# Kernel tuning notes

Hardware: AMD Instinct MI355X
Metric: run time of the kernel (lower is better)

## Reference

```python
import jax, jax.numpy as jnp
import numpy as np

NUM_HEADS = 8
LN_EPS = 1e-6


def _layer_norm(x, gamma, beta):
    mu = jnp.mean(x, axis=-1, keepdims=True)
    var = jnp.mean(jnp.square(x - mu), axis=-1, keepdims=True)
    return (x - mu) / jnp.sqrt(var + LN_EPS) * gamma + beta


def setup_inputs() -> dict:
    key = jax.random.key(0)
    B, S, H, F = 4, 2048, 1024, 4096
    ks = jax.random.split(key, 12)
    scale = 1.0 / np.sqrt(H)
    x = jax.random.normal(ks[0], (B, S, H), dtype=jnp.float32)
    # additive padding mask: 1 where masked, 0 where attended
    mask = jax.random.randint(ks[1], (B, 1, 1, S), 0, 2).astype(jnp.float32)
    Wq = jax.random.normal(ks[2], (H, H), dtype=jnp.float32) * scale
    Wk = jax.random.normal(ks[3], (H, H), dtype=jnp.float32) * scale
    Wv = jax.random.normal(ks[4], (H, H), dtype=jnp.float32) * scale
    Wo = jax.random.normal(ks[5], (H, H), dtype=jnp.float32) * scale
    W1 = jax.random.normal(ks[6], (H, F), dtype=jnp.float32) * scale
    b1 = jnp.zeros((F,), dtype=jnp.float32)
    W2 = jax.random.normal(ks[7], (F, H), dtype=jnp.float32) * (1.0 / np.sqrt(F))
    b2 = jnp.zeros((H,), dtype=jnp.float32)
    gamma = jnp.ones((H,), dtype=jnp.float32)
    beta = jnp.zeros((H,), dtype=jnp.float32)
    return {"x": x, "mask": mask, "Wq": Wq, "Wk": Wk, "Wv": Wv, "Wo": Wo,
            "W1": W1, "b1": b1, "W2": W2, "b2": b2, "gamma": gamma, "beta": beta}


def reference(x, mask, Wq, Wk, Wv, Wo, W1, b1, W2, b2, gamma, beta):
    B, S, H = x.shape
    nh = NUM_HEADS
    d = H // nh

    def split_heads(t):
        return t.reshape(B, S, nh, d).transpose(0, 2, 1, 3)  # [B,nh,S,d]

    q = split_heads(x @ Wq)
    k = split_heads(x @ Wk)
    v = split_heads(x @ Wv)

    # FAITHFUL to source bug: score /= d**(-0.5)  ==  score * sqrt(d)
    scores = jnp.einsum('bhqd,bhkd->bhqk', q, k) * jnp.sqrt(jnp.float32(d))
    scores = scores + mask * (-1e9)
    attn = jax.nn.softmax(scores, axis=-1)
    ctx = jnp.einsum('bhqk,bhkd->bhqd', attn, v)
    ctx = ctx.transpose(0, 2, 1, 3).reshape(B, S, H)
    attn_out = ctx @ Wo

    # dropout = identity (eval mode)
    x = _layer_norm(x + attn_out, gamma, beta)
    ffn = jnp.maximum(x @ W1 + b1, 0.0) @ W2 + b2
    x = _layer_norm(x + ffn, gamma, beta)
    return x
```

## Files before the change

### kernel.cpp

```cpp
#include <hip/hip_runtime.h>


typedef __bf16 bf16;
typedef __bf16 bf16x4 __attribute__((ext_vector_type(4)));
typedef __bf16 bf16x8 __attribute__((ext_vector_type(8)));
typedef float  f32x4  __attribute__((ext_vector_type(4)));

#define MFMA16(a, b, c) __builtin_amdgcn_mfma_f32_16x16x32_bf16(a, b, c, 0, 0, 0)

typedef const __attribute__((address_space(1))) void* gas_cptr;
typedef __attribute__((address_space(3))) void* las_ptr;

__device__ __forceinline__ void g2l16(const void* g, void* l) {
    __builtin_amdgcn_global_load_lds((gas_cptr)g, (las_ptr)l, 16, 0, 0);
}

__device__ __forceinline__ uint b16bits(bf16 v) {
    union { bf16 h; unsigned short u; } cv; cv.h = v; return (uint)cv.u;
}

__device__ __forceinline__ int xcd_swz(int d, int nwg) {
    return (d & 7) * (nwg >> 3) + (d >> 3);
}

__global__ __launch_bounds__(256) void split_f32_k(
    const float* __restrict__ in, bf16* __restrict__ hi, bf16* __restrict__ lo)
{
    const long i = (long)blockIdx.x * 256 + threadIdx.x;
    const float4 v = *(const float4*)(in + i * 4);
    const float a[4] = {v.x, v.y, v.z, v.w};
    bf16x4 h, l;
#pragma unroll
    for (int j = 0; j < 4; j++) {
        h[j] = (bf16)a[j];
        l[j] = (bf16)(a[j] - (float)h[j]);
    }
    *(bf16x4*)(hi + i * 4) = h;
    *(bf16x4*)(lo + i * 4) = l;
}

__global__ __launch_bounds__(256) void mask_scan_k(
    const float* __restrict__ mask, unsigned short* __restrict__ cidx,
    int* __restrict__ nbuf)
{
    __shared__ int wsum[4];
    const int b = blockIdx.x, t = threadIdx.x;
    const int lane = t & 63, w = t >> 6;
    float m[8];
    *(float4*)&m[0] = *(const float4*)(mask + b * 2048 + t * 8);
    *(float4*)&m[4] = *(const float4*)(mask + b * 2048 + t * 8 + 4);
    int keep[8], cnt = 0;
#pragma unroll
    for (int j = 0; j < 8; j++) {
        keep[j] = (m[j] < 0.5f) ? 1 : 0;
        cnt += keep[j];
    }
    int pre = cnt;
#pragma unroll
    for (int off = 1; off < 64; off <<= 1) {
        const int nv = __shfl_up(pre, off);
        if (lane >= off) pre += nv;
    }
    if (lane == 63) wsum[w] = pre;
    __syncthreads();
    int base = 0;
    for (int i = 0; i < w; i++) base += wsum[i];
    const int total = wsum[0] + wsum[1] + wsum[2] + wsum[3];
    int p = base + pre - cnt;
#pragma unroll
    for (int j = 0; j < 8; j++)
        if (keep[j]) cidx[b * 2048 + (p++)] = (unsigned short)(t * 8 + j);
    for (int j = t; j < 2048; j += 256)
        if (j >= total) cidx[b * 2048 + j] = 0;
    if (t == 0) nbuf[b] = total;
}

__global__ __launch_bounds__(256) void transpose_f32_k(
    const float* __restrict__ in, bf16* __restrict__ out_hi, bf16* __restrict__ out_lo,
    int in_rs, int out_rs)
{
    __shared__ uint Th[64][33];
    __shared__ uint Tl[64][33];
    const long c0 = (long)blockIdx.x * 64;
    const long r0 = (long)blockIdx.y * 64;
    const int t = threadIdx.x, rp = t >> 3, cc = t & 7;
    const float* pa = in + (r0 + 2 * rp) * (long)in_rs + c0 + cc * 8;
    const float* pb = pa + in_rs;
    float a[8], b[8];
    *(float4*)&a[0] = *(const float4*)pa;
    *(float4*)&a[4] = *(const float4*)(pa + 4);
    *(float4*)&b[0] = *(const float4*)pb;
    *(float4*)&b[4] = *(const float4*)(pb + 4);
#pragma unroll
    for (int j = 0; j < 8; j++) {
        const bf16 ah = (bf16)a[j], bh = (bf16)b[j];
        Th[cc * 8 + j][rp] = b16bits(ah) | (b16bits(bh) << 16);
        const bf16 al = (bf16)(a[j] - (float)ah), bl = (bf16)(b[j] - (float)bh);
        Tl[cc * 8 + j][rp] = b16bits(al) | (b16bits(bl) << 16);
    }
    __syncthreads();
#pragma unroll
    for (int i = 0; i < 2; i++) {
        const int task = i * 256 + t;
        const int c = task >> 3, ch = task & 7;
        uint4 wv;
        wv.x = Th[c][ch * 4 + 0]; wv.y = Th[c][ch * 4 + 1];
        wv.z = Th[c][ch * 4 + 2]; wv.w = Th[c][ch * 4 + 3];
        *(uint4*)(out_hi + (c0 + c) * (long)out_rs + r0 + ch * 8) = wv;
        if (out_lo) {
            uint4 wl;
            wl.x = Tl[c][ch * 4 + 0]; wl.y = Tl[c][ch * 4 + 1];
            wl.z = Tl[c][ch * 4 + 2]; wl.w = Tl[c][ch * 4 + 3];
            *(uint4*)(out_lo + (c0 + c) * (long)out_rs + r0 + ch * 8) = wl;
        }
    }
}

__global__ __launch_bounds__(256) void transpose_bf16_k(
    const bf16* __restrict__ in, bf16* __restrict__ out,
    int in_rs, int out_rs, int nh, long bo_in, long bi_in, long bo_out,
    const int* __restrict__ nbuf)
{
    __shared__ uint T[64][33];
    const int z = blockIdx.z;
    const int bb = z / nh;
    const long r0 = (long)blockIdx.y * 64;
    if (nbuf) {
        const int npad = (nbuf[bb] + 63) & ~63;
        if (r0 >= npad) return;
    }
    const bf16* inp = in + (long)bb * bo_in + (long)(z % nh) * bi_in;
    bf16* outp = out + (long)z * bo_out;
    const long c0 = (long)blockIdx.x * 64;
    const int t = threadIdx.x, rp = t >> 3, cc = t & 7;

    const uint4 ra = *(const uint4*)(inp + (r0 + 2 * rp) * (long)in_rs + c0 + cc * 8);
    const uint4 rb = *(const uint4*)(inp + (r0 + 2 * rp + 1) * (long)in_rs + c0 + cc * 8);
    const uint a32[4] = {ra.x, ra.y, ra.z, ra.w};
    const uint b32[4] = {rb.x, rb.y, rb.z, rb.w};
#pragma unroll
    for (int j = 0; j < 8; j++) {
        const uint av = (j & 1) ? (a32[j >> 1] >> 16) : (a32[j >> 1] & 0xffffu);
        const uint bv = (j & 1) ? (b32[j >> 1] >> 16) : (b32[j >> 1] & 0xffffu);
        T[cc * 8 + j][rp] = av | (bv << 16);
    }
    __syncthreads();
#pragma unroll
    for (int i = 0; i < 2; i++) {
        const int task = i * 256 + t;
        const int c = task >> 3, ch = task & 7;
        uint4 wv;
        wv.x = T[c][ch * 4 + 0]; wv.y = T[c][ch * 4 + 1];
        wv.z = T[c][ch * 4 + 2]; wv.w = T[c][ch * 4 + 3];
        *(uint4*)(outp + (c0 + c) * (long)out_rs + r0 + ch * 8) = wv;
    }
}

__global__ __launch_bounds__(256) void gemm_bf16_k(
    const bf16* __restrict__ A, const bf16* __restrict__ Bt,
    bf16* __restrict__ out,
    const float* __restrict__ bias, int relu, int M, int N, int K,
    const unsigned short* __restrict__ cidx, const int* __restrict__ nbuf)
{
    __shared__ __align__(16) bf16 As[128 * 32];
    __shared__ __align__(16) bf16 Bs[128 * 32];
    const int t = threadIdx.x;
    const int fr = t & 15, fq = (t >> 4) & 3;
    const int w = t >> 6, wm = w & 1, wn = w >> 1;
    const int nx = gridDim.x;
    const int d = xcd_swz(blockIdx.y * nx + blockIdx.x, nx * gridDim.y);
    const long mBase = (long)(d / nx) * 128;
    const long nBase = (long)(d % nx) * 128;

    const int arow = t >> 2;
    const int akc  = (t & 3) * 8;
    long r0 = mBase + arow, r1 = r0 + 64;
    if (cidx) {
        const int b = (int)(mBase >> 11);
        const int npad = (nbuf[b] + 63) & ~63;
        if ((int)(mBase & 2047) >= npad) return;
        r0 = (long)b * 2048 + cidx[b * 2048 + (int)(r0 & 2047)];
        r1 = (long)b * 2048 + cidx[b * 2048 + (int)(r1 & 2047)];
    }

    f32x4 acc[4][4];
#pragma unroll
    for (int i = 0; i < 4; i++)
#pragma unroll
        for (int j = 0; j < 4; j++) acc[i][j] = (f32x4){0.f, 0.f, 0.f, 0.f};

    const bf16* ga0 = A + r0 * (long)K + akc;
    const bf16* ga1 = A + r1 * (long)K + akc;
    const bf16* gb0 = Bt + (nBase + arow) * (long)K + akc;
    const bf16* gb1 = Bt + (nBase + arow + 64) * (long)K + akc;
    bf16* la0 = &As[t * 8];
    bf16* la1 = &As[(256 + t) * 8];
    bf16* lb0 = &Bs[t * 8];
    bf16* lb1 = &Bs[(256 + t) * 8];

    const int aoff = (wm * 64 + fr) * 32 + fq * 8;
    const int boff = (wn * 64 + fr) * 32 + fq * 8;

    for (int kt = 0; kt < K; kt += 32) {
        g2l16(ga0 + kt, la0);
        g2l16(ga1 + kt, la1);
        g2l16(gb0 + kt, lb0);
        g2l16(gb1 + kt, lb1);
        __syncthreads();
        bf16x8 af[4], bfv[4];
#pragma unroll
        for (int mt = 0; mt < 4; mt++) af[mt] = *(const bf16x8*)&As[aoff + mt * 512];
#pragma unroll
        for (int nt = 0; nt < 4; nt++) bfv[nt] = *(const bf16x8*)&Bs[boff + nt * 512];
#pragma unroll
        for (int mt = 0; mt < 4; mt++)
#pragma unroll
            for (int nt = 0; nt < 4; nt++)
                acc[mt][nt] = MFMA16(af[mt], bfv[nt], acc[mt][nt]);
        __syncthreads();
    }

    const long crow0 = mBase + wm * 64;
    const long ccol0 = nBase + wn * 64;
#pragma unroll
    for (int nt = 0; nt < 4; nt++) {
        const long col = ccol0 + nt * 16 + fr;
        const float bv = bias ? bias[col] : 0.0f;
#pragma unroll
        for (int mt = 0; mt < 4; mt++)
#pragma unroll
            for (int r = 0; r < 4; r++) {
                const long rowg = crow0 + mt * 16 + fq * 4 + r;
                float v = acc[mt][nt][r] + bv;
                if (relu) v = fmaxf(v, 0.0f);
                out[rowg * (long)N + col] = (bf16)v;
            }
    }
}

__global__ __launch_bounds__(256) void gemm_qk_split_k(
    const bf16* __restrict__ Ah, const bf16* __restrict__ Al,
    const bf16* __restrict__ BhQ, const bf16* __restrict__ BlQ,
    bf16* __restrict__ qhi, bf16* __restrict__ qlo,
    const bf16* __restrict__ BhK, const bf16* __restrict__ BlK,
    bf16* __restrict__ khi, bf16* __restrict__ klo,
    int M, int N, int K,
    const unsigned short* __restrict__ cidx, const int* __restrict__ nbuf)
{
    __shared__ __align__(16) bf16 Ahs[128 * 32];
    __shared__ __align__(16) bf16 Als[128 * 32];
    __shared__ __align__(16) bf16 Bhs[128 * 32];
    __shared__ __align__(16) bf16 Bls[128 * 32];
    const int t = threadIdx.x;
    const int fr = t & 15, fq = (t >> 4) & 3;
    const int w = t >> 6, wm = w & 1, wn = w >> 1;
    const int nx = gridDim.x;
    const int nxy = nx * gridDim.y;
    const int dAll = xcd_swz(blockIdx.z * nxy + blockIdx.y * nx + blockIdx.x, nxy * 2);
    const int z = dAll / nxy;
    const int d = dAll - z * nxy;
    const long mBase = (long)(d / nx) * 128;
    const long nBase = (long)(d % nx) * 128;

    const bf16* Bh = z ? BhK : BhQ;
    const bf16* Bl = z ? BlK : BlQ;
    bf16* out_hi = z ? khi : qhi;
    bf16* out_lo = z ? klo : qlo;

    const int arow = t >> 2;
    const int akc  = (t & 3) * 8;
    long r0 = mBase + arow, r1 = r0 + 64;
    if (z) {
        const int b = (int)(mBase >> 11);
        const int npad = (nbuf[b] + 63) & ~63;
        if ((int)(mBase & 2047) >= npad) return;
        r0 = (long)b * 2048 + cidx[b * 2048 + (int)(r0 & 2047)];
        r1 = (long)b * 2048 + cidx[b * 2048 + (int)(r1 & 2047)];
    }

    f32x4 acc[4][4];
#pragma unroll
    for (int i = 0; i < 4; i++)
#pragma unroll
        for (int j = 0; j < 4; j++) acc[i][j] = (f32x4){0.f, 0.f, 0.f, 0.f};

    const long ga0 = r0 * (long)K + akc;
    const long ga1 = r1 * (long)K + akc;
    const long gb0 = (nBase + arow) * (long)K + akc;
    const long gb1 = (nBase + arow + 64) * (long)K + akc;

    const int aoff = (wm * 64 + fr) * 32 + fq * 8;
    const int boff = (wn * 64 + fr) * 32 + fq * 8;

    for (int kt = 0; kt < K; kt += 32) {
        g2l16(Ah + ga0 + kt, &Ahs[t * 8]);
        g2l16(Ah + ga1 + kt, &Ahs[(256 + t) * 8]);
        g2l16(Al + ga0 + kt, &Als[t * 8]);
        g2l16(Al + ga1 + kt, &Als[(256 + t) * 8]);
        g2l16(Bh + gb0 + kt, &Bhs[t * 8]);
        g2l16(Bh + gb1 + kt, &Bhs[(256 + t) * 8]);
        g2l16(Bl + gb0 + kt, &Bls[t * 8]);
        g2l16(Bl + gb1 + kt, &Bls[(256 + t) * 8]);
        __syncthreads();
        bf16x8 ah[4], al[4], bh[4], bl[4];
#pragma unroll
        for (int mt = 0; mt < 4; mt++) {
            ah[mt] = *(const bf16x8*)&Ahs[aoff + mt * 512];
            al[mt] = *(const bf16x8*)&Als[aoff + mt * 512];
        }
#pragma unroll
        for (int nt = 0; nt < 4; nt++) {
            bh[nt] = *(const bf16x8*)&Bhs[boff + nt * 512];
            bl[nt] = *(const bf16x8*)&Bls[boff + nt * 512];
        }
#pragma unroll
        for (int mt = 0; mt < 4; mt++)
#pragma unroll
            for (int nt = 0; nt < 4; nt++) {
                acc[mt][nt] = MFMA16(ah[mt], bh[nt], acc[mt][nt]);
                acc[mt][nt] = MFMA16(ah[mt], bl[nt], acc[mt][nt]);
                acc[mt][nt] = MFMA16(al[mt], bh[nt], acc[mt][nt]);
            }
        __syncthreads();
    }

    const long crow0 = mBase + wm * 64;
    const long ccol0 = nBase + wn * 64;
#pragma unroll
    for (int nt = 0; nt < 4; nt++) {
        const long col = ccol0 + nt * 16 + fr;
#pragma unroll
        for (int mt = 0; mt < 4; mt++)
#pragma unroll
            for (int r = 0; r < 4; r++) {
                const long rowg = crow0 + mt * 16 + fq * 4 + r;
                const float v = acc[mt][nt][r];
                const long idx = rowg * (long)N + col;
                const bf16 h = (bf16)v;
                out_hi[idx] = h;
                out_lo[idx] = (bf16)(v - (float)h);
            }
    }
}

#define KROW 132
#define VROW 68
#define PROW 68
__global__ __launch_bounds__(256, 2) void flash_attn_k(
    const bf16* __restrict__ qhi, const bf16* __restrict__ qlo,
    const bf16* __restrict__ khi, const bf16* __restrict__ klo,
    const bf16* __restrict__ vt, const int* __restrict__ nbuf,
    bf16* __restrict__ ctx)
{
    __shared__ __align__(16) bf16 Kh[64 * KROW];
    __shared__ __align__(16) bf16 Kl[64 * KROW];
    __shared__ __align__(16) bf16 Vs[128 * VROW];
    bf16* PsB = Kl;
    const float scale = 11.3137085f;
    const int t = threadIdx.x, w = t >> 6;
    const int fr = t & 15, fq = (t >> 4) & 3;
    const int blk = xcd_swz(blockIdx.x, 512);
    const int qt = blk & 15, bh_ = blk >> 4, b = bh_ >> 3, h = bh_ & 7;
    const int qrow0 = qt * 128 + w * 16;

    const int nB = nbuf[b];
    const int ntiles = (nB + 63) >> 6;

    bf16x8 qh[2][4], ql[2][4];
#pragma unroll
    for (int mt = 0; mt < 2; mt++) {
        const long qoff = ((long)(b * 2048 + qrow0 + mt * 64 + fr)) * 1024 + h * 128 + fq * 8;
#pragma unroll
        for (int s = 0; s < 4; s++) {
            qh[mt][s] = *(const bf16x8*)(qhi + qoff + s * 32);
            ql[mt][s] = *(const bf16x8*)(qlo + qoff + s * 32);
        }
    }
    f32x4 o[2][8];
#pragma unroll
    for (int mt = 0; mt < 2; mt++)
#pragma unroll
        for (int nt = 0; nt < 8; nt++) o[mt][nt] = (f32x4){0.f, 0.f, 0.f, 0.f};
    float m_run[2][4], l_run[2][4];
#pragma unroll
    for (int mt = 0; mt < 2; mt++)
#pragma unroll
        for (int r = 0; r < 4; r++) { m_run[mt][r] = -1e30f; l_run[mt][r] = 0.f; }

    const long kbase = (long)(b * 2048) * 1024 + h * 128 + (long)(t & 15) * 8;
    const long vbase = ((long)bh_ * 128) * 2048 + (long)(t & 7) * 8;

    for (int kt = 0; kt < ntiles; kt++) {
        __syncthreads();
#pragma unroll
        for (int i = 0; i < 4; i++) {
            const int key = i * 16 + (t >> 4);
            const long g = kbase + (long)(kt * 64 + key) * 1024;
            const bf16x8 vk_h = *(const bf16x8*)(khi + g);
            const bf16x8 vk_l = *(const bf16x8*)(klo + g);
            const int d = i * 32 + (t >> 3);
            const bf16x8 vv = *(const bf16x8*)(vt + vbase + (long)d * 2048 + kt * 64);
            *(bf16x8*)&Kh[key * KROW + (t & 15) * 8] = vk_h;
            *(bf16x8*)&Kl[key * KROW + (t & 15) * 8] = vk_l;
            *(bf16x8*)&Vs[d * VROW + (t & 7) * 8] = vv;
        }
        float madd[4];
#pragma unroll
        for (int ct = 0; ct < 4; ct++)
            madd[ct] = (kt * 64 + ct * 16 + fr < nB) ? 0.0f : -1e9f;
        __syncthreads();

        f32x4 sc[2][4];
#pragma unroll
        for (int mt = 0; mt < 2; mt++)
#pragma unroll
            for (int ct = 0; ct < 4; ct++) sc[mt][ct] = (f32x4){0.f, 0.f, 0.f, 0.f};
        __builtin_amdgcn_s_setprio(1);
#pragma unroll
        for (int s = 0; s < 4; s++)
#pragma unroll
            for (int ct = 0; ct < 4; ct++) {
                const int off = (ct * 16 + fr) * KROW + s * 32 + fq * 8;
                const bf16x8 kh8 = *(const bf16x8*)&Kh[off];
                const bf16x8 kl8 = *(const bf16x8*)&Kl[off];
#pragma unroll
                for (int mt = 0; mt < 2; mt++) {
                    sc[mt][ct] = MFMA16(qh[mt][s], kh8, sc[mt][ct]);
                    sc[mt][ct] = MFMA16(qh[mt][s], kl8, sc[mt][ct]);
                    sc[mt][ct] = MFMA16(ql[mt][s], kh8, sc[mt][ct]);
                }
            }
        __builtin_amdgcn_s_setprio(0);
        __syncthreads();

#pragma unroll
        for (int mt = 0; mt < 2; mt++) {
            float alpha[4];
#pragma unroll
            for (int r = 0; r < 4; r++) {
                float mx = sc[mt][0][r] * scale + madd[0];
                mx = fmaxf(mx, sc[mt][1][r] * scale + madd[1]);
                mx = fmaxf(mx, sc[mt][2][r] * scale + madd[2]);
                mx = fmaxf(mx, sc[mt][3][r] * scale + madd[3]);
                mx = fmaxf(mx, __shfl_xor(mx, 1));
                mx = fmaxf(mx, __shfl_xor(mx, 2));
                mx = fmaxf(mx, __shfl_xor(mx, 4));
                mx = fmaxf(mx, __shfl_xor(mx, 8));
                const float mn = fmaxf(m_run[mt][r], mx);
                alpha[r] = __expf(m_run[mt][r] - mn);
                m_run[mt][r] = mn;
            }
            float lt[4] = {0.f, 0.f, 0.f, 0.f};
#pragma unroll
            for (int ct = 0; ct < 4; ct++)
#pragma unroll
                for (int r = 0; r < 4; r++) {
                    const float p = __expf(sc[mt][ct][r] * scale + madd[ct] - m_run[mt][r]);
                    lt[r] += p;
                    PsB[(w * 16 + fq * 4 + r) * PROW + ct * 16 + fr] = (bf16)p;
                }
#pragma unroll
            for (int r = 0; r < 4; r++) {
                float s_ = lt[r];
                s_ += __shfl_xor(s_, 1); s_ += __shfl_xor(s_, 2);
                s_ += __shfl_xor(s_, 4); s_ += __shfl_xor(s_, 8);
                l_run[mt][r] = l_run[mt][r] * alpha[r] + s_;
            }
            const int need = (alpha[0] < 1.f) | (alpha[1] < 1.f) |
                             (alpha[2] < 1.f) | (alpha[3] < 1.f);
            if (__any(need)) {
#pragma unroll
                for (int nt = 0; nt < 8; nt++)
#pragma unroll
                    for (int r = 0; r < 4; r++) o[mt][nt][r] *= alpha[r];
            }

            __builtin_amdgcn_s_setprio(1);
#pragma unroll
            for (int sp = 0; sp < 2; sp++) {
                const bf16x8 pf = *(const bf16x8*)&PsB[(w * 16 + fr) * PROW + sp * 32 + fq * 8];
#pragma unroll
                for (int nt = 0; nt < 8; nt++) {
                    const bf16x8 vf = *(const bf16x8*)&Vs[(nt * 16 + fr) * VROW + sp * 32 + fq * 8];
                    o[mt][nt] = MFMA16(pf, vf, o[mt][nt]);
                }
            }
            __builtin_amdgcn_s_setprio(0);
        }
    }
#pragma unroll
    for (int mt = 0; mt < 2; mt++)
#pragma unroll
        for (int r = 0; r < 4; r++) {
            const float inv = l_run[mt][r] > 0.f ? 1.0f / l_run[mt][r] : 0.f;
#pragma unroll
            for (int nt = 0; nt < 8; nt++) {
                const long idx = ((long)(b * 2048 + qrow0 + mt * 64 + fq * 4 + r)) * 1024
                               + h * 128 + nt * 16 + fr;
                ctx[idx] = (bf16)(o[mt][nt][r] * inv);
            }
        }
}

__global__ __launch_bounds__(256) void add_ln_k(
    const float* __restrict__ xf, const bf16* __restrict__ y,
    const float* __restrict__ gamma, const float* __restrict__ beta,
    float* __restrict__ out, bf16* __restrict__ out_b)
{
    __shared__ float red[8];
    const long row = blockIdx.x;
    const int t = threadIdx.x, lane = t & 63, w = t >> 6;
    float v[4];
    const float4 xv = *(const float4*)(xf + row * 1024 + t * 4);
    v[0] = xv.x; v[1] = xv.y; v[2] = xv.z; v[3] = xv.w;
    const bf16x4 yv = *(const bf16x4*)(y + row * 1024 + t * 4);
    float s = 0.f, s2 = 0.f;
#pragma unroll
    for (int i = 0; i < 4; i++) {
        v[i] += (float)yv[i];
        s += v[i]; s2 += v[i] * v[i];
    }
#pragma unroll
    for (int off = 1; off < 64; off <<= 1) {
        s += __shfl_xor(s, off);
        s2 += __shfl_xor(s2, off);
    }
    if (lane == 0) { red[w] = s; red[4 + w] = s2; }
    __syncthreads();
    s = red[0] + red[1] + red[2] + red[3];
    s2 = red[4] + red[5] + red[6] + red[7];
    const float mean = s * (1.0f / 1024.0f);
    const float var = s2 * (1.0f / 1024.0f) - mean * mean;
    const float rstd = rsqrtf(var + 1e-6f);
    float4 ov;
    ov.x = (v[0] - mean) * rstd * gamma[t * 4 + 0] + beta[t * 4 + 0];
    ov.y = (v[1] - mean) * rstd * gamma[t * 4 + 1] + beta[t * 4 + 1];
    ov.z = (v[2] - mean) * rstd * gamma[t * 4 + 2] + beta[t * 4 + 2];
    ov.w = (v[3] - mean) * rstd * gamma[t * 4 + 3] + beta[t * 4 + 3];
    *(float4*)(out + row * 1024 + t * 4) = ov;
    if (out_b) {
        bf16x4 hb;
        hb[0] = (bf16)ov.x; hb[1] = (bf16)ov.y; hb[2] = (bf16)ov.z; hb[3] = (bf16)ov.w;
        *(bf16x4*)(out_b + row * 1024 + t * 4) = hb;
    }
}

extern "C" void kernel_launch(void* const* d_in, const int* in_sizes, int n_in,
                              void* d_out, int out_size, void* d_ws, size_t ws_size,
                              hipStream_t stream)
{
    (void)in_sizes; (void)n_in; (void)out_size; (void)ws_size;
    const float* x     = (const float*)d_in[0];
    const float* mask  = (const float*)d_in[1];
    const float* Wq    = (const float*)d_in[2];
    const float* Wk    = (const float*)d_in[3];
    const float* Wv    = (const float*)d_in[4];
    const float* Wo    = (const float*)d_in[5];
    const float* W1    = (const float*)d_in[6];
    const float* b1    = (const float*)d_in[7];
    const float* W2    = (const float*)d_in[8];
    const float* b2    = (const float*)d_in[9];
    const float* gamma = (const float*)d_in[10];
    const float* beta  = (const float*)d_in[11];
    float* out = (float*)d_out;

    char* ws = (char*)d_ws;
    const size_t SZ = 8192ul * 1024 * 2;
    bf16* qhi  = (bf16*)(ws + 0 * SZ);
    bf16* qlo  = (bf16*)(ws + 1 * SZ);
    bf16* khi  = (bf16*)(ws + 2 * SZ);
    bf16* klo  = (bf16*)(ws + 3 * SZ);
    bf16* hbuf = (bf16*)(ws + 0 * SZ);
    bf16* vbuf = (bf16*)(ws + 4 * SZ);
    bf16* ctxb = vbuf;
    bf16* vtb  = (bf16*)(ws + 5 * SZ);
    bf16* fbuf = vtb;
    bf16* xh   = (bf16*)(ws + 6 * SZ);
    bf16* xl   = (bf16*)(ws + 7 * SZ);
    bf16* aob  = xl;
    float* x1f = (float*)(ws + 8 * SZ);
    bf16* x1b  = (bf16*)(ws + 10 * SZ);
    char* wts  = ws + 11 * SZ;
    bf16* Wqth = (bf16*)(wts);
    bf16* Wqtl = (bf16*)(wts + 1 * 2097152);
    bf16* Wkth = (bf16*)(wts + 2 * 2097152);
    bf16* Wktl = (bf16*)(wts + 3 * 2097152);
    bf16* Wvt  = (bf16*)(wts + 4 * 2097152);
    bf16* Wot  = (bf16*)(wts + 5 * 2097152);
    bf16* W1t  = (bf16*)(wts + 6 * 2097152);
    bf16* W2t  = (bf16*)(wts + 6 * 2097152 + 8388608);
    unsigned short* cidxb = (unsigned short*)(wts + 6 * 2097152 + 2 * 8388608);
    int* nbuf = (int*)((char*)cidxb + 4 * 2048 * sizeof(unsigned short));

    const dim3 blk(256);
    split_f32_k<<<dim3(8192), blk, 0, stream>>>(x, xh, xl);
    mask_scan_k<<<dim3(4), blk, 0, stream>>>(mask, cidxb, nbuf);
    transpose_f32_k<<<dim3(16, 16), blk, 0, stream>>>(Wq, Wqth, Wqtl, 1024, 1024);
    transpose_f32_k<<<dim3(16, 16), blk, 0, stream>>>(Wk, Wkth, Wktl, 1024, 1024);
    transpose_f32_k<<<dim3(16, 16), blk, 0, stream>>>(Wv, Wvt, nullptr, 1024, 1024);
    transpose_f32_k<<<dim3(16, 16), blk, 0, stream>>>(Wo, Wot, nullptr, 1024, 1024);
    transpose_f32_k<<<dim3(64, 16), blk, 0, stream>>>(W1, W1t, nullptr, 4096, 1024);
    transpose_f32_k<<<dim3(16, 64), blk, 0, stream>>>(W2, W2t, nullptr, 1024, 4096);
    gemm_qk_split_k<<<dim3(8, 64, 2), blk, 0, stream>>>(
        xh, xl, Wqth, Wqtl, qhi, qlo, Wkth, Wktl, khi, klo,
        8192, 1024, 1024, cidxb, nbuf);
    gemm_bf16_k<<<dim3(8, 64), blk, 0, stream>>>(xh, Wvt, vbuf, nullptr, 0, 8192, 1024, 1024,
                                                 cidxb, nbuf);
    transpose_bf16_k<<<dim3(2, 32, 32), blk, 0, stream>>>(vbuf, vtb, 1024, 2048, 8,
                                                          (long)2048 * 1024, 128L, (long)128 * 2048,
                                                          nbuf);
    flash_attn_k<<<dim3(512), blk, 0, stream>>>(qhi, qlo, khi, klo, vtb, nbuf, ctxb);
    gemm_bf16_k<<<dim3(8, 64), blk, 0, stream>>>(ctxb, Wot, aob, nullptr, 0, 8192, 1024, 1024,
                                                 nullptr, nullptr);
    add_ln_k<<<dim3(8192), blk, 0, stream>>>(x, aob, gamma, beta, x1f, x1b);
    gemm_bf16_k<<<dim3(32, 64), blk, 0, stream>>>(x1b, W1t, hbuf, b1, 1, 8192, 4096, 1024,
                                                  nullptr, nullptr);
    gemm_bf16_k<<<dim3(8, 64), blk, 0, stream>>>(hbuf, W2t, fbuf, b2, 0, 8192, 1024, 4096,
                                                 nullptr, nullptr);
    add_ln_k<<<dim3(8192), blk, 0, stream>>>(x1f, fbuf, gamma, beta, out, nullptr);
}
```

Baseline: 660.8 us.

## Fuse V projection into split QK GEMM launch and give attention its own P buffer

After: 669.4 us. About the same (+1.3%).

```diff
diff --git a/kernel.cpp b/kernel.cpp
--- a/kernel.cpp
+++ b/kernel.cpp
@@ -238,12 +238,13 @@
     }
 }
 
-__global__ __launch_bounds__(256) void gemm_qk_split_k(
+__global__ __launch_bounds__(256) void gemm_qkv_k(
     const bf16* __restrict__ Ah, const bf16* __restrict__ Al,
     const bf16* __restrict__ BhQ, const bf16* __restrict__ BlQ,
     bf16* __restrict__ qhi, bf16* __restrict__ qlo,
     const bf16* __restrict__ BhK, const bf16* __restrict__ BlK,
     bf16* __restrict__ khi, bf16* __restrict__ klo,
+    const bf16* __restrict__ Bv, bf16* __restrict__ vout,
     int M, int N, int K,
     const unsigned short* __restrict__ cidx, const int* __restrict__ nbuf)
 {
@@ -256,21 +257,22 @@
     const int w = t >> 6, wm = w & 1, wn = w >> 1;
     const int nx = gridDim.x;
     const int nxy = nx * gridDim.y;
-    const int dAll = xcd_swz(blockIdx.z * nxy + blockIdx.y * nx + blockIdx.x, nxy * 2);
+    const int dAll = xcd_swz(blockIdx.z * nxy + blockIdx.y * nx + blockIdx.x, nxy * 3);
     const int z = dAll / nxy;
     const int d = dAll - z * nxy;
     const long mBase = (long)(d / nx) * 128;
     const long nBase = (long)(d % nx) * 128;
 
-    const bf16* Bh = z ? BhK : BhQ;
-    const bf16* Bl = z ? BlK : BlQ;
-    bf16* out_hi = z ? khi : qhi;
-    bf16* out_lo = z ? klo : qlo;
+    const bf16* Bh = (z == 0) ? BhQ : ((z == 1) ? BhK : Bv);
+    const bf16* Bl = (z == 0) ? BlQ : BlK;
+    bf16* out_hi = (z == 0) ? qhi : ((z == 1) ? khi : vout);
+    bf16* out_lo = (z == 0) ? qlo : klo;
+    const bool splitp = (z < 2);
 
     const int arow = t >> 2;
     const int akc  = (t & 3) * 8;
     long r0 = mBase + arow, r1 = r0 + 64;
-    if (z) {
+    if (z >= 1) {
         const int b = (int)(mBase >> 11);
         const int npad = (nbuf[b] + 63) & ~63;
         if ((int)(mBase & 2047) >= npad) return;
@@ -295,32 +297,41 @@
     for (int kt = 0; kt < K; kt += 32) {
         g2l16(Ah + ga0 + kt, &Ahs[t * 8]);
         g2l16(Ah + ga1 + kt, &Ahs[(256 + t) * 8]);
-        g2l16(Al + ga0 + kt, &Als[t * 8]);
-        g2l16(Al + ga1 + kt, &Als[(256 + t) * 8]);
         g2l16(Bh + gb0 + kt, &Bhs[t * 8]);
         g2l16(Bh + gb1 + kt, &Bhs[(256 + t) * 8]);
-        g2l16(Bl + gb0 + kt, &Bls[t * 8]);
-        g2l16(Bl + gb1 + kt, &Bls[(256 + t) * 8]);
+        if (splitp) {
+            g2l16(Al + ga0 + kt, &Als[t * 8]);
+            g2l16(Al + ga1 + kt, &Als[(256 + t) * 8]);
+            g2l16(Bl + gb0 + kt, &Bls[t * 8]);
+            g2l16(Bl + gb1 + kt, &Bls[(256 + t) * 8]);
+        }
         __syncthreads();
-        bf16x8 ah[4], al[4], bh[4], bl[4];
-#pragma unroll
-        for (int mt = 0; mt < 4; mt++) {
-            ah[mt] = *(const bf16x8*)&Ahs[aoff + mt * 512];
-            al[mt] = *(const bf16x8*)&Als[aoff + mt * 512];
+        bf16x8 ah[4], bh[4];
+#pragma unroll
+        for (int mt = 0; mt < 4; mt++) ah[mt] = *(const bf16x8*)&Ahs[aoff + mt * 512];
+#pragma unroll
+        for (int nt = 0; nt < 4; nt++) bh[nt] = *(const bf16x8*)&Bhs[boff + nt * 512];
+        if (splitp) {
+            bf16x8 al[4], bl[4];
+#pragma unroll
+            for (int mt = 0; mt < 4; mt++) al[mt] = *(const bf16x8*)&Als[aoff + mt * 512];
+#pragma unroll
+            for (int nt = 0; nt < 4; nt++) bl[nt] = *(const bf16x8*)&Bls[boff + nt * 512];
+#pragma unroll
+            for (int mt = 0; mt < 4; mt++)
+#pragma unroll
+                for (int nt = 0; nt < 4; nt++) {
+                    acc[mt][nt] = MFMA16(ah[mt], bh[nt], acc[mt][nt]);
+                    acc[mt][nt] = MFMA16(ah[mt], bl[nt], acc[mt][nt]);
+                    acc[mt][nt] = MFMA16(al[mt], bh[nt], acc[mt][nt]);
+                }
+        } else {
+#pragma unroll
+            for (int mt = 0; mt < 4; mt++)
+#pragma unroll
+                for (int nt = 0; nt < 4; nt++)
+                    acc[mt][nt] = MFMA16(ah[mt], bh[nt], acc[mt][nt]);
         }
-#pragma unroll
-        for (int nt = 0; nt < 4; nt++) {
-            bh[nt] = *(const bf16x8*)&Bhs[boff + nt * 512];
-            bl[nt] = *(const bf16x8*)&Bls[boff + nt * 512];
-        }
-#pragma unroll
-        for (int mt = 0; mt < 4; mt++)
-#pragma unroll
-            for (int nt = 0; nt < 4; nt++) {
-                acc[mt][nt] = MFMA16(ah[mt], bh[nt], acc[mt][nt]);
-                acc[mt][nt] = MFMA16(ah[mt], bl[nt], acc[mt][nt]);
-                acc[mt][nt] = MFMA16(al[mt], bh[nt], acc[mt][nt]);
-            }
         __syncthreads();
     }
 
@@ -338,7 +349,7 @@
                 const long idx = rowg * (long)N + col;
                 const bf16 h = (bf16)v;
                 out_hi[idx] = h;
-                out_lo[idx] = (bf16)(v - (float)h);
+                if (splitp) out_lo[idx] = (bf16)(v - (float)h);
             }
     }
 }
@@ -355,7 +366,7 @@
     __shared__ __align__(16) bf16 Kh[64 * KROW];
     __shared__ __align__(16) bf16 Kl[64 * KROW];
     __shared__ __align__(16) bf16 Vs[128 * VROW];
-    bf16* PsB = Kl;
+    __shared__ __align__(16) bf16 Ps[4][16 * PROW];
     const float scale = 11.3137085f;
     const int t = threadIdx.x, w = t >> 6;
     const int fr = t & 15, fq = (t >> 4) & 3;
@@ -431,7 +442,6 @@
                 }
             }
         __builtin_amdgcn_s_setprio(0);
-        __syncthreads();
 
 #pragma unroll
         for (int mt = 0; mt < 2; mt++) {
@@ -457,7 +467,7 @@
                 for (int r = 0; r < 4; r++) {
                     const float p = __expf(sc[mt][ct][r] * scale + madd[ct] - m_run[mt][r]);
                     lt[r] += p;
-                    PsB[(w * 16 + fq * 4 + r) * PROW + ct * 16 + fr] = (bf16)p;
+                    Ps[w][(fq * 4 + r) * PROW + ct * 16 + fr] = (bf16)p;
                 }
 #pragma unroll
             for (int r = 0; r < 4; r++) {
@@ -478,7 +488,7 @@
             __builtin_amdgcn_s_setprio(1);
 #pragma unroll
             for (int sp = 0; sp < 2; sp++) {
-                const bf16x8 pf = *(const bf16x8*)&PsB[(w * 16 + fr) * PROW + sp * 32 + fq * 8];
+                const bf16x8 pf = *(const bf16x8*)&Ps[w][fr * PROW + sp * 32 + fq * 8];
 #pragma unroll
                 for (int nt = 0; nt < 8; nt++) {
                     const bf16x8 vf = *(const bf16x8*)&Vs[(nt * 16 + fr) * VROW + sp * 32 + fq * 8];
@@ -601,11 +611,9 @@
     transpose_f32_k<<<dim3(16, 16), blk, 0, stream>>>(Wo, Wot, nullptr, 1024, 1024);
     transpose_f32_k<<<dim3(64, 16), blk, 0, stream>>>(W1, W1t, nullptr, 4096, 1024);
     transpose_f32_k<<<dim3(16, 64), blk, 0, stream>>>(W2, W2t, nullptr, 1024, 4096);
-    gemm_qk_split_k<<<dim3(8, 64, 2), blk, 0, stream>>>(
-        xh, xl, Wqth, Wqtl, qhi, qlo, Wkth, Wktl, khi, klo,
+    gemm_qkv_k<<<dim3(8, 64, 3), blk, 0, stream>>>(
+        xh, xl, Wqth, Wqtl, qhi, qlo, Wkth, Wktl, khi, klo, Wvt, vbuf,
         8192, 1024, 1024, cidxb, nbuf);
-    gemm_bf16_k<<<dim3(8, 64), blk, 0, stream>>>(xh, Wvt, vbuf, nullptr, 0, 8192, 1024, 1024,
-                                                 cidxb, nbuf);
     transpose_bf16_k<<<dim3(2, 32, 32), blk, 0, stream>>>(vbuf, vtb, 1024, 2048, 8,
                                                           (long)2048 * 1024, 128L, (long)128 * 2048,
                                                           nbuf);
```
